# Kernel tuning notes

Measured on AMD Instinct MI355X. Metric: run time of the kernel, lower is better.

Reference implementation:

```python
import jax, jax.numpy as jnp
import numpy as np

B, N, M, C1, C2 = 16, 4096, 1024, 128, 256
MLP0, MLP1 = 256, 256
IN_CH = C1 + C2
EPS = 1e-5


def setup_inputs() -> dict:
    key = jax.random.key(0)
    ks = jax.random.split(key, 6)
    return {
        "xyz1": jax.random.normal(ks[0], (B, 3, N), jnp.float32),
        "xyz2": jax.random.normal(ks[1], (B, 3, M), jnp.float32),
        "points1": jax.random.normal(ks[2], (B, C1, N), jnp.float32),
        "points2": jax.random.normal(ks[3], (B, C2, M), jnp.float32),
        "W1": jax.random.normal(ks[4], (MLP0, IN_CH), jnp.float32) * (1.0 / np.sqrt(IN_CH)),
        "gamma1": jnp.ones((MLP0,), jnp.float32),
        "beta1": jnp.zeros((MLP0,), jnp.float32),
        "W2": jax.random.normal(ks[5], (MLP1, MLP0), jnp.float32) * (1.0 / np.sqrt(MLP0)),
        "gamma2": jnp.ones((MLP1,), jnp.float32),
        "beta2": jnp.zeros((MLP1,), jnp.float32),
    }


def _batchnorm(x, gamma, beta):
    # x: (B, N, C); normalize per channel over batch*length (training-mode BN, biased var)
    mean = jnp.mean(x, axis=(0, 1))
    var = jnp.mean((x - mean) ** 2, axis=(0, 1))
    return (x - mean) * jax.lax.rsqrt(var + EPS) * gamma + beta


def reference(xyz1, xyz2, points1, points2, W1, gamma1, beta1, W2, gamma2, beta2):
    p1 = jnp.swapaxes(xyz1, 1, 2)  # (B, N, 3)
    p2 = jnp.swapaxes(xyz2, 1, 2)  # (B, M, 3)
    # squared pairwise distances (B, N, M); squaring preserves 3-NN ordering,
    # and the original squares the euclidean dist before weighting anyway
    d2 = jnp.sum((p1[:, :, None, :] - p2[:, None, :, :]) ** 2, axis=-1)
    neg_d2, idx = jax.lax.top_k(-d2, 3)  # 3 smallest distances
    dist2 = jnp.maximum(-neg_d2, 1e-10)  # (B, N, 3)
    inv = 1.0 / dist2
    weight = inv / jnp.sum(inv, axis=-1, keepdims=True)  # (B, N, 3)
    f2 = jnp.swapaxes(points2, 1, 2)  # (B, M, C2)
    b, n, k = idx.shape
    gathered = jnp.take_along_axis(
        f2, idx.reshape(b, n * k)[:, :, None], axis=1
    ).reshape(b, n, k, -1)  # (B, N, 3, C2)
    interp = jnp.einsum("bnk,bnkc->bnc", weight, gathered)  # (B, N, C2)
    feat = jnp.concatenate([interp, jnp.swapaxes(points1, 1, 2)], axis=-1)  # (B, N, C1+C2)
    h = jnp.einsum("bnc,oc->bno", feat, W1)  # conv1d k=1, no bias
    h = jax.nn.relu(_batchnorm(h, gamma1, beta1))
    h = jnp.einsum("bnc,oc->bno", h, W2)
    h = jax.nn.relu(_batchnorm(h, gamma2, beta2))
    return jnp.swapaxes(h, 1, 2)  # (B, MLP1, N), channel-first like torch
```

## Files before the change

kernel.cpp:

```cpp
#include <hip/hip_runtime.h>

typedef unsigned short u16;
typedef unsigned int u32;

#define BB 16
#define NN 4096
#define MM 1024
#define C1V 128
#define C2V 256
#define EPSV 1e-5f
#define INV_CNT (1.0f/65536.0f)
#define NREP 32

typedef __attribute__((ext_vector_type(8))) short bf16x8;
typedef __attribute__((ext_vector_type(4))) float f32x4;

static __device__ __forceinline__ u16 f2b(float f) {
  u32 u = __float_as_uint(f);
  u32 r = (u + 0x7FFFu + ((u >> 16) & 1u)) >> 16;
  return (u16)r;
}
static __device__ __forceinline__ float b2f(u16 s) {
  return __uint_as_float(((u32)s) << 16);
}

#define GLD_LDS16(gp, lp)                                                      \
  __builtin_amdgcn_global_load_lds(                                            \
      (const __attribute__((address_space(1))) void*)(gp),                     \
      (__attribute__((address_space(3))) void*)(lp), 16, 0, 0)

__device__ __forceinline__ void tcast_tile64(const float* __restrict__ in,
                                             u16* __restrict__ out, int C,
                                             int P, int p0, int c0, int b,
                                             float (*tile)[33]) {
  int tx = threadIdx.x & 31, ty = threadIdx.x >> 5;
  const float* ib = in + (size_t)b * C * P;
  u16* ob = out + (size_t)b * P * C;
#pragma unroll
  for (int i = 0; i < 8; ++i)
    tile[ty + i * 8][tx] = ib[(size_t)(c0 + ty + i * 8) * P + p0 + tx];
  __syncthreads();
#pragma unroll
  for (int i = 0; i < 4; ++i) {
    int p = ty + i * 8;
    u32 v = (u32)f2b(tile[tx * 2][p]) | ((u32)f2b(tile[tx * 2 + 1][p]) << 16);
    *(u32*)&ob[(size_t)(p0 + p) * C + c0 + tx * 2] = v;
  }
}

__global__ __launch_bounds__(256) void prep_kernel(
    const float* __restrict__ xyz1, const float* __restrict__ xyz2,
    float* __restrict__ pd, int* __restrict__ pi,
    const float* __restrict__ points1, const float* __restrict__ points2,
    u16* __restrict__ p1t, u16* __restrict__ p2t,
    const float* __restrict__ W1, const float* __restrict__ W2,
    u16* __restrict__ W1b, u16* __restrict__ W2b,
    float* __restrict__ statsZero) {
  __shared__ float4 cand[256];
  __shared__ float tile[64][33];
  int bx = blockIdx.x;
  int t = threadIdx.x;

  if (bx < 512) {
    int c = bx & 3;
    int qt = (bx >> 2) & 7;
    int b = bx >> 5;
    const float* x2b = xyz2 + b * 3 * MM;
    {
      float x = x2b[c * 256 + t];
      float y = x2b[MM + c * 256 + t];
      float z = x2b[2 * MM + c * 256 + t];
      cand[t] = make_float4(x, y, z, x * x + y * y + z * z);
    }
    __syncthreads();
    const float* x1b = xyz1 + b * 3 * NN;
    int n0 = qt * 512 + t;
    int n1 = n0 + 256;
    float px0 = x1b[n0], py0 = x1b[NN + n0], pz0 = x1b[2 * NN + n0];
    float px1 = x1b[n1], py1 = x1b[NN + n1], pz1 = x1b[2 * NN + n1];
    const float INF = 3.4e38f;
    float k00 = INF, k01 = INF, k02 = INF;
    float k10 = INF, k11 = INF, k12 = INF;
    int j00 = 0, j01 = 0, j02 = 0;
    int j10 = 0, j11 = 0, j12 = 0;
#pragma unroll 8
    for (int m = 0; m < 256; ++m) {
      float4 cd = cand[m];
      {
        float dot = fmaf(px0, cd.x, fmaf(py0, cd.y, pz0 * cd.z));
        float key = fmaf(-2.0f, dot, cd.w);
        bool c0 = key < k00, c1 = key < k01, c2 = key < k02;
        k02 = c1 ? k01 : (c2 ? key : k02);
        j02 = c1 ? j01 : (c2 ? m : j02);
        k01 = c0 ? k00 : (c1 ? key : k01);
        j01 = c0 ? j00 : (c1 ? m : j01);
        k00 = c0 ? key : k00;
        j00 = c0 ? m : j00;
      }
      {
        float dot = fmaf(px1, cd.x, fmaf(py1, cd.y, pz1 * cd.z));
        float key = fmaf(-2.0f, dot, cd.w);
        bool c0 = key < k10, c1 = key < k11, c2 = key < k12;
        k12 = c1 ? k11 : (c2 ? key : k12);
        j12 = c1 ? j11 : (c2 ? m : j12);
        k11 = c0 ? k10 : (c1 ? key : k11);
        j11 = c0 ? j10 : (c1 ? m : j11);
        k10 = c0 ? key : k10;
        j10 = c0 ? m : j10;
      }
    }
    float pn0 = px0 * px0 + py0 * py0 + pz0 * pz0;
    float pn1 = px1 * px1 + py1 * py1 + pz1 * pz1;
    int gq0 = b * NN + n0;
    int gq1 = b * NN + n1;
    int base = c << 8;
    ((float4*)pd)[(size_t)c * 65536 + gq0] =
        make_float4(fmaxf(k00 + pn0, 1e-10f), fmaxf(k01 + pn0, 1e-10f),
                    fmaxf(k02 + pn0, 1e-10f), 0.0f);
    ((int4*)pi)[(size_t)c * 65536 + gq0] =
        make_int4(base + j00, base + j01, base + j02, 0);
    ((float4*)pd)[(size_t)c * 65536 + gq1] =
        make_float4(fmaxf(k10 + pn1, 1e-10f), fmaxf(k11 + pn1, 1e-10f),
                    fmaxf(k12 + pn1, 1e-10f), 0.0f);
    ((int4*)pi)[(size_t)c * 65536 + gq1] =
        make_int4(base + j10, base + j11, base + j12, 0);
  } else if (bx < 1152) {
    int i = (bx - 512) * 256 + t;
    if (i < 98304) W1b[i] = f2b(W1[i]);
    else if (i < 163840) W2b[i - 98304] = f2b(W2[i - 98304]);
  } else if (bx < 1184) {
    ((float4*)statsZero)[(bx - 1152) * 256 + t] =
        make_float4(0.f, 0.f, 0.f, 0.f);
  } else if (bx < 3232) {
    int local = bx - 1184;
    int pt = local & 31, ct = (local >> 5) & 3, b = local >> 7;
    tcast_tile64(points2, p2t, C2V, MM, pt * 32, ct * 64, b, tile);
  } else {
    int local = bx - 3232;
    int pt = local & 127, ct = (local >> 7) & 1, b = local >> 8;
    tcast_tile64(points1, p1t, C1V, NN, pt * 32, ct * 64, b, tile);
  }
}

template <int K, int NTILES, bool OUTB>
__global__ __launch_bounds__(256) void gemm_mfma(
    const u16* __restrict__ A, int lda, const u16* __restrict__ B, int ldb,
    void* __restrict__ out) {
  __shared__ u16 smem[16384];
  int t = threadIdx.x;
  int w = t >> 6, l = t & 63;
  int n0;
  if (NTILES > 0) {
    int p = blockIdx.x;
    int batch = ((p & 7) << 1) | ((p >> 3) & 1);
    int nt = p >> 4;
    n0 = (batch * NTILES + nt) * 128;
  } else {
    n0 = blockIdx.x * 128;
  }
  int o0 = blockIdx.y * 128;

  int wm = w & 1, wn = w >> 1;
  int lr = l >> 2, lc = l & 3;
  int q = l >> 4, m = l & 15;

  f32x4 acc[4][4] = {};
  u16* As = smem;
  u16* Bs = smem + 4096;

  const u16* arow = A + (size_t)n0 * lda;
  const u16* brow = B + (size_t)o0 * ldb;

#pragma unroll
  for (int kt = 0; kt < K; kt += 32) {
    __syncthreads();
#pragma unroll
    for (int r = 0; r < 2; ++r) {
      int row = r * 64 + w * 16 + lr;
      GLD_LDS16(arow + (size_t)row * lda + kt + lc * 8, As + row * 32 + lc * 8);
    }
#pragma unroll
    for (int r = 0; r < 2; ++r) {
      int row = r * 64 + w * 16 + lr;
      GLD_LDS16(brow + (size_t)row * ldb + kt + lc * 8, Bs + row * 32 + lc * 8);
    }
    __syncthreads();
    bf16x8 af[4], bf[4];
#pragma unroll
    for (int i = 0; i < 4; ++i)
      af[i] = *(const bf16x8*)(As + (wm * 64 + i * 16 + m) * 32 + q * 8);
#pragma unroll
    for (int j = 0; j < 4; ++j)
      bf[j] = *(const bf16x8*)(Bs + (wn * 64 + j * 16 + m) * 32 + q * 8);
#pragma unroll
    for (int i = 0; i < 4; ++i)
#pragma unroll
      for (int j = 0; j < 4; ++j)
        acc[i][j] =
            __builtin_amdgcn_mfma_f32_16x16x32_bf16(af[i], bf[j], acc[i][j], 0, 0, 0);
  }

  if (OUTB) {
    __syncthreads();
#pragma unroll
    for (int i = 0; i < 4; ++i)
#pragma unroll
      for (int reg = 0; reg < 4; ++reg) {
        int row = wm * 64 + i * 16 + q * 4 + reg;
#pragma unroll
        for (int j = 0; j < 4; ++j)
          smem[row * 128 + wn * 64 + j * 16 + m] = f2b(acc[i][j][reg]);
      }
    __syncthreads();
    u16* outp = (u16*)out;
    int rbase = w * 32 + (l >> 4);
    int seg = l & 15;
#pragma unroll
    for (int itr = 0; itr < 8; ++itr) {
      int row = rbase + itr * 4;
      uint4 v = *(const uint4*)(smem + row * 128 + seg * 8);
      *(uint4*)(outp + (size_t)(n0 + row) * 256 + o0 + seg * 8) = v;
    }
  } else {
#pragma unroll
    for (int i = 0; i < 4; ++i) {
      int gr = n0 + wm * 64 + i * 16 + q * 4;
#pragma unroll
      for (int reg = 0; reg < 4; ++reg)
#pragma unroll
        for (int j = 0; j < 4; ++j) {
          int gc = o0 + wn * 64 + j * 16 + m;
          ((float*)out)[(size_t)(gr + reg) * 256 + gc] = acc[i][j][reg];
        }
    }
  }
}

__global__ __launch_bounds__(256) void gemm1_64(
    const u16* __restrict__ A, const u16* __restrict__ B,
    u16* __restrict__ out, const u16* __restrict__ G,
    const float* __restrict__ pd, const int* __restrict__ pi,
    float* __restrict__ statsOut) {
  __shared__ __align__(16) u16 smem[16384];
  __shared__ float wsh[64][3];
  __shared__ int ish[64][3];
  int t = threadIdx.x;
  int w = t >> 6, l = t & 63;
  int p = blockIdx.x;
  int batch = ((p & 7) << 1) | ((p >> 3) & 1);
  int nt = p >> 4;
  int n0 = batch * NN + nt * 64;

  if (t < 64) {
    int gq = n0 + t;
    float4 d0 = ((const float4*)pd)[gq];
    int4 ii0 = ((const int4*)pi)[gq];
    float a0 = d0.x, a1 = d0.y, a2 = d0.z;
    int b0 = ii0.x, b1 = ii0.y, b2 = ii0.z;
#pragma unroll
    for (int c = 1; c < 4; ++c) {
      float4 dc = ((const float4*)pd)[(size_t)c * 65536 + gq];
      int4 ic = ((const int4*)pi)[(size_t)c * 65536 + gq];
      float kv[3] = {dc.x, dc.y, dc.z};
      int jv[3] = {ic.x, ic.y, ic.z};
#pragma unroll
      for (int j = 0; j < 3; ++j) {
        float key = kv[j];
        int idx = jv[j];
        bool c0 = key < a0, c1 = key < a1, c2 = key < a2;
        a2 = c1 ? a1 : (c2 ? key : a2);
        b2 = c1 ? b1 : (c2 ? idx : b2);
        a1 = c0 ? a0 : (c1 ? key : a1);
        b1 = c0 ? b0 : (c1 ? idx : b1);
        a0 = c0 ? key : a0;
        b0 = c0 ? idx : b0;
      }
    }
    float v0 = 1.0f / a0, v1 = 1.0f / a1, v2 = 1.0f / a2;
    float s = 1.0f / (v0 + v1 + v2);
    wsh[t][0] = v0 * s; wsh[t][1] = v1 * s; wsh[t][2] = v2 * s;
    ish[t][0] = b0;     ish[t][1] = b1;     ish[t][2] = b2;
  }

  int q = l >> 4, m = l & 15;
  int sr = l >> 2, lc = l & 3;

  f32x4 acc[4][4] = {};
  u16* As = smem;
  u16* Bs = smem + 2048;
  const u16* arow = A + (size_t)n0 * 128;

#pragma unroll
  for (int kt = 0; kt < 128; kt += 32) {
    __syncthreads();
    {
      int row = w * 16 + sr;
      GLD_LDS16(arow + (size_t)row * 128 + kt + lc * 8, As + row * 32 + lc * 8);
    }
#pragma unroll
    for (int r = 0; r < 4; ++r) {
      int row = r * 64 + w * 16 + sr;
      GLD_LDS16(B + (size_t)row * 384 + kt + lc * 8, Bs + row * 32 + lc * 8);
    }
    __syncthreads();
    bf16x8 af[4], bf[4];
#pragma unroll
    for (int i = 0; i < 4; ++i)
      af[i] = *(const bf16x8*)(As + (i * 16 + m) * 32 + q * 8);
#pragma unroll
    for (int j = 0; j < 4; ++j)
      bf[j] = *(const bf16x8*)(Bs + (w * 64 + j * 16 + m) * 32 + q * 8);
#pragma unroll
    for (int i = 0; i < 4; ++i)
#pragma unroll
      for (int j = 0; j < 4; ++j)
        acc[i][j] =
            __builtin_amdgcn_mfma_f32_16x16x32_bf16(af[i], bf[j], acc[i][j], 0, 0, 0);
  }

  __syncthreads();
  {
    int b = n0 >> 12;
    int rl = t >> 2, qt = t & 3;
    float w0 = wsh[rl][0], w1 = wsh[rl][1], w2 = wsh[rl][2];
    const u16* g0 = G + ((size_t)(b * 1024 + ish[rl][0])) * 256 + qt * 64;
    const u16* g1 = G + ((size_t)(b * 1024 + ish[rl][1])) * 256 + qt * 64;
    const u16* g2 = G + ((size_t)(b * 1024 + ish[rl][2])) * 256 + qt * 64;
    int r3 = rl & 7;
#pragma unroll
    for (int c8 = 0; c8 < 8; ++c8) {
      bf16x8 v0 = *(const bf16x8*)(g0 + c8 * 8);
      bf16x8 v1 = *(const bf16x8*)(g1 + c8 * 8);
      bf16x8 v2 = *(const bf16x8*)(g2 + c8 * 8);
      union { uint4 u; u16 s[8]; } o;
#pragma unroll
      for (int e = 0; e < 8; ++e) {
        float f = w0 * b2f((u16)v0[e]) + w1 * b2f((u16)v1[e]) +
                  w2 * b2f((u16)v2[e]);
        o.s[e] = f2b(f);
      }
      int ch = (qt * 8 + c8) ^ r3;
      *(uint4*)(smem + rl * 256 + ch * 8) = o.u;
    }
  }
  __syncthreads();
#pragma unroll
  for (int i = 0; i < 4; ++i)
#pragma unroll
    for (int reg = 0; reg < 4; ++reg) {
      int row = i * 16 + q * 4 + reg;
      int rx = row & 7;
#pragma unroll
      for (int j = 0; j < 4; ++j) {
        int col = w * 64 + j * 16 + m;
        int off = row * 256 + (((col >> 3) ^ rx) << 3) + (col & 7);
        acc[i][j][reg] += b2f(smem[off]);
      }
    }

  {
    int rep = blockIdx.x & (NREP - 1);
#pragma unroll
    for (int j = 0; j < 4; ++j) {
      float s = 0.0f, ss = 0.0f;
#pragma unroll
      for (int i = 0; i < 4; ++i)
#pragma unroll
        for (int reg = 0; reg < 4; ++reg) {
          float v = acc[i][j][reg];
          s += v;
          ss += v * v;
        }
      s += __shfl_down(s, 32); ss += __shfl_down(ss, 32);
      s += __shfl_down(s, 16); ss += __shfl_down(ss, 16);
      if (l < 16) {
        int c = w * 64 + j * 16 + l;
        atomicAdd(&statsOut[rep * 512 + c], s);
        atomicAdd(&statsOut[rep * 512 + 256 + c], ss);
      }
    }
  }

  __syncthreads();
#pragma unroll
  for (int i = 0; i < 4; ++i)
#pragma unroll
    for (int reg = 0; reg < 4; ++reg) {
      int row = i * 16 + q * 4 + reg;
#pragma unroll
      for (int j = 0; j < 4; ++j)
        smem[row * 256 + w * 64 + j * 16 + m] = f2b(acc[i][j][reg]);
    }
  __syncthreads();
  int rbase = t >> 5, seg = t & 31;
#pragma unroll
  for (int itr = 0; itr < 8; ++itr) {
    int row = rbase + itr * 8;
    uint4 v = *(const uint4*)(smem + row * 256 + seg * 8);
    *(uint4*)(out + (size_t)(n0 + row) * 256 + seg * 8) = v;
  }
}

__global__ __launch_bounds__(256) void gemm2_64(
    const u16* __restrict__ A, const u16* __restrict__ B,
    u16* __restrict__ out, float* __restrict__ statsOut,
    const float* __restrict__ statsInR, const float* __restrict__ gamma,
    const float* __restrict__ beta) {
  __shared__ __align__(16) u16 smem[16384];
  __shared__ float scA[256], shA[256];
  int t = threadIdx.x;
  int w = t >> 6, l = t & 63;
  int n0 = blockIdx.x * 64;

  {
    float s = 0.0f, qq = 0.0f;
#pragma unroll
    for (int r = 0; r < NREP; ++r) {
      s += statsInR[r * 512 + t];
      qq += statsInR[r * 512 + 256 + t];
    }
    float mean = s * INV_CNT;
    float var = qq * INV_CNT - mean * mean;
    float sc = rsqrtf(var + EPSV) * gamma[t];
    scA[t] = sc;
    shA[t] = beta[t] - mean * sc;
  }

  int q = l >> 4, m = l & 15;
  int sr = l >> 2, lc = l & 3;

  f32x4 acc[4][4] = {};
  u16* As = smem;
  u16* Bs = smem + 2048;
  const u16* arow = A + (size_t)n0 * 256;

#pragma unroll
  for (int kt = 0; kt < 256; kt += 32) {
    __syncthreads();
    {
      int row = w * 16 + sr;
      union { uint4 u; u16 s[8]; } v, o;
      v.u = *(const uint4*)(arow + (size_t)row * 256 + kt + lc * 8);
      int cb = kt + lc * 8;
#pragma unroll
      for (int j = 0; j < 8; ++j) {
        float f = fmaf(b2f(v.s[j]), scA[cb + j], shA[cb + j]);
        o.s[j] = f2b(fmaxf(f, 0.0f));
      }
      *(uint4*)(As + row * 32 + lc * 8) = o.u;
    }
#pragma unroll
    for (int r = 0; r < 4; ++r) {
      int row = r * 64 + w * 16 + sr;
      GLD_LDS16(B + (size_t)row * 256 + kt + lc * 8, Bs + row * 32 + lc * 8);
    }
    __syncthreads();
    bf16x8 af[4], bf[4];
#pragma unroll
    for (int i = 0; i < 4; ++i)
      af[i] = *(const bf16x8*)(As + (i * 16 + m) * 32 + q * 8);
#pragma unroll
    for (int j = 0; j < 4; ++j)
      bf[j] = *(const bf16x8*)(Bs + (w * 64 + j * 16 + m) * 32 + q * 8);
#pragma unroll
    for (int i = 0; i < 4; ++i)
#pragma unroll
      for (int j = 0; j < 4; ++j)
        acc[i][j] =
            __builtin_amdgcn_mfma_f32_16x16x32_bf16(af[i], bf[j], acc[i][j], 0, 0, 0);
  }

  {
    int rep = blockIdx.x & (NREP - 1);
#pragma unroll
    for (int j = 0; j < 4; ++j) {
      float s = 0.0f, ss = 0.0f;
#pragma unroll
      for (int i = 0; i < 4; ++i)
#pragma unroll
        for (int reg = 0; reg < 4; ++reg) {
          float v = acc[i][j][reg];
          s += v;
          ss += v * v;
        }
      s += __shfl_down(s, 32); ss += __shfl_down(ss, 32);
      s += __shfl_down(s, 16); ss += __shfl_down(ss, 16);
      if (l < 16) {
        int c = w * 64 + j * 16 + l;
        atomicAdd(&statsOut[rep * 512 + c], s);
        atomicAdd(&statsOut[rep * 512 + 256 + c], ss);
      }
    }
  }

  __syncthreads();
#pragma unroll
  for (int i = 0; i < 4; ++i)
#pragma unroll
    for (int reg = 0; reg < 4; ++reg) {
      int row = i * 16 + q * 4 + reg;
#pragma unroll
      for (int j = 0; j < 4; ++j)
        smem[row * 256 + w * 64 + j * 16 + m] = f2b(acc[i][j][reg]);
    }
  __syncthreads();
  int rbase = t >> 5, seg = t & 31;
#pragma unroll
  for (int itr = 0; itr < 8; ++itr) {
    int row = rbase + itr * 8;
    uint4 v = *(const uint4*)(smem + row * 256 + seg * 8);
    *(uint4*)(out + (size_t)(n0 + row) * 256 + seg * 8) = v;
  }
}

__global__ __launch_bounds__(256) void bn2t_kernel(
    const u16* __restrict__ h2, const float* __restrict__ statsR,
    const float* __restrict__ gamma, const float* __restrict__ beta,
    float* __restrict__ out) {
  __shared__ float tile[64][65];
  __shared__ float sS[64], sH[64];
  int t = threadIdx.x;
  int n0 = blockIdx.x * 64, c0 = blockIdx.y * 64, b = blockIdx.z;
  if (t < 64) {
    int c = c0 + t;
    float s = 0.0f, qq = 0.0f;
#pragma unroll
    for (int r = 0; r < NREP; ++r) {
      s += statsR[r * 512 + c];
      qq += statsR[r * 512 + 256 + c];
    }
    float mean = s * INV_CNT;
    float var = qq * INV_CNT - mean * mean;
    float sc = rsqrtf(var + EPSV) * gamma[c];
    sS[t] = sc;
    sH[t] = beta[c] - mean * sc;
  }
  __syncthreads();
  int tx = t & 15, ty = t >> 4;
#pragma unroll
  for (int i = 0; i < 4; ++i) {
    int n = ty + i * 16;
    uint2 v = *(const uint2*)(h2 + ((size_t)b * NN + n0 + n) * 256 + c0 + tx * 4);
    int c = tx * 4;
    tile[n][c + 0] = fmaxf(fmaf(b2f((u16)(v.x & 0xffff)), sS[c + 0], sH[c + 0]), 0.0f);
    tile[n][c + 1] = fmaxf(fmaf(b2f((u16)(v.x >> 16)),    sS[c + 1], sH[c + 1]), 0.0f);
    tile[n][c + 2] = fmaxf(fmaf(b2f((u16)(v.y & 0xffff)), sS[c + 2], sH[c + 2]), 0.0f);
    tile[n][c + 3] = fmaxf(fmaf(b2f((u16)(v.y >> 16)),    sS[c + 3], sH[c + 3]), 0.0f);
  }
  __syncthreads();
#pragma unroll
  for (int i = 0; i < 4; ++i) {
    int c = ty + i * 16;
    int nq = tx * 4;
    float4 o4 = make_float4(tile[nq + 0][c], tile[nq + 1][c],
                            tile[nq + 2][c], tile[nq + 3][c]);
    *(float4*)(out + ((size_t)(b * 256 + c0 + c)) * NN + n0 + nq) = o4;
  }
}

extern "C" void kernel_launch(void* const* d_in, const int* in_sizes, int n_in,
                              void* d_out, int out_size, void* d_ws,
                              size_t ws_size, hipStream_t stream) {
  const float* xyz1    = (const float*)d_in[0];
  const float* xyz2    = (const float*)d_in[1];
  const float* points1 = (const float*)d_in[2];
  const float* points2 = (const float*)d_in[3];
  const float* W1      = (const float*)d_in[4];
  const float* gamma1  = (const float*)d_in[5];
  const float* beta1   = (const float*)d_in[6];
  const float* W2      = (const float*)d_in[7];
  const float* gamma2  = (const float*)d_in[8];
  const float* beta2   = (const float*)d_in[9];

  char* ws = (char*)d_ws;
  float* stats1R = (float*)(ws + 0);
  float* stats2R = (float*)(ws + 65536);
  u16*   W1b     = (u16*)(ws + 131072);
  u16*   W2b     = (u16*)(ws + 327680);
  u16*   p2t     = (u16*)(ws + 458752);
  u16*   p1t     = (u16*)(ws + 8847360);
  u16*   G       = (u16*)(ws + 25624576);
  u16*   h2b     = (u16*)(ws + 34013184);
  float* pd      = (float*)(ws + 67567616);
  int*   pi      = (int*)(ws + 71761920);
  u16*   h1b     = (u16*)d_out;
  float* out     = (float*)d_out;

  prep_kernel<<<7328, 256, 0, stream>>>(xyz1, xyz2, pd, pi, points1, points2,
                                        p1t, p2t, W1, W2, W1b, W2b, stats1R);
  gemm_mfma<256, 8, true><<<dim3(128, 2), 256, 0, stream>>>(p2t, 256, W1b, 384,
                                                            G);
  gemm1_64<<<1024, 256, 0, stream>>>(p1t, W1b + 256, h1b, G, pd, pi, stats1R);
  gemm2_64<<<1024, 256, 0, stream>>>(h1b, W2b, h2b, stats2R, stats1R, gamma1,
                                     beta1);
  bn2t_kernel<<<dim3(64, 4, 16), 256, 0, stream>>>(h2b, stats2R, gamma2,
                                                   beta2, out);
}
```

Measured before the change: 221.8 us.

## Move KNN search blocks from prep kernel into the first GEMM launch

The 3-nearest-neighbour search blocks leave the prep kernel and run as extra blocks (blockIdx.x >= 128) of the first MFMA GEMM launch, reusing its shared memory for the candidate array. The GEMM grid grows from 128x2 to 384x2 to cover the 512 KNN blocks. KNN only depends on xyz inputs, so it can overlap with the p2t·W1 GEMM instead of sharing the prep launch with the cast/transpose work. The risk is that KNN blocks and GEMM blocks compete for CUs and that the prep kernel, now lighter, no longer hides the KNN compute.

After: 225.2 us. About the same (+1.5%).

```diff
diff --git a/kernel.cpp b/kernel.cpp
--- a/kernel.cpp
+++ b/kernel.cpp
@@ -49,22 +49,48 @@
 }
 
 __global__ __launch_bounds__(256) void prep_kernel(
-    const float* __restrict__ xyz1, const float* __restrict__ xyz2,
-    float* __restrict__ pd, int* __restrict__ pi,
     const float* __restrict__ points1, const float* __restrict__ points2,
     u16* __restrict__ p1t, u16* __restrict__ p2t,
     const float* __restrict__ W1, const float* __restrict__ W2,
     u16* __restrict__ W1b, u16* __restrict__ W2b,
     float* __restrict__ statsZero) {
-  __shared__ float4 cand[256];
   __shared__ float tile[64][33];
   int bx = blockIdx.x;
   int t = threadIdx.x;
 
-  if (bx < 512) {
-    int c = bx & 3;
-    int qt = (bx >> 2) & 7;
-    int b = bx >> 5;
+  if (bx < 640) {
+    int i = bx * 256 + t;
+    if (i < 98304) W1b[i] = f2b(W1[i]);
+    else if (i < 163840) W2b[i - 98304] = f2b(W2[i - 98304]);
+  } else if (bx < 672) {
+    ((float4*)statsZero)[(bx - 640) * 256 + t] =
+        make_float4(0.f, 0.f, 0.f, 0.f);
+  } else if (bx < 2720) {
+    int local = bx - 672;
+    int pt = local & 31, ct = (local >> 5) & 3, b = local >> 7;
+    tcast_tile64(points2, p2t, C2V, MM, pt * 32, ct * 64, b, tile);
+  } else {
+    int local = bx - 2720;
+    int pt = local & 127, ct = (local >> 7) & 1, b = local >> 8;
+    tcast_tile64(points1, p1t, C1V, NN, pt * 32, ct * 64, b, tile);
+  }
+}
+
+template <int K, int NTILES, bool OUTB, bool KNN>
+__global__ __launch_bounds__(256) void gemm_mfma(
+    const u16* __restrict__ A, int lda, const u16* __restrict__ B, int ldb,
+    void* __restrict__ out, const float* __restrict__ xyz1,
+    const float* __restrict__ xyz2, float* __restrict__ pd,
+    int* __restrict__ pi) {
+  __shared__ __align__(16) u16 smem[16384];
+  int t = threadIdx.x;
+
+  if (KNN && blockIdx.x >= 128) {
+    float4* cand = (float4*)smem;
+    int id = (int)(blockIdx.x - 128) | ((int)blockIdx.y << 8);
+    int c = id & 3;
+    int qt = (id >> 2) & 7;
+    int b = id >> 5;
     const float* x2b = xyz2 + b * 3 * MM;
     {
       float x = x2b[c * 256 + t];
@@ -124,30 +150,9 @@
                     fmaxf(k12 + pn1, 1e-10f), 0.0f);
     ((int4*)pi)[(size_t)c * 65536 + gq1] =
         make_int4(base + j10, base + j11, base + j12, 0);
-  } else if (bx < 1152) {
-    int i = (bx - 512) * 256 + t;
-    if (i < 98304) W1b[i] = f2b(W1[i]);
-    else if (i < 163840) W2b[i - 98304] = f2b(W2[i - 98304]);
-  } else if (bx < 1184) {
-    ((float4*)statsZero)[(bx - 1152) * 256 + t] =
-        make_float4(0.f, 0.f, 0.f, 0.f);
-  } else if (bx < 3232) {
-    int local = bx - 1184;
-    int pt = local & 31, ct = (local >> 5) & 3, b = local >> 7;
-    tcast_tile64(points2, p2t, C2V, MM, pt * 32, ct * 64, b, tile);
-  } else {
-    int local = bx - 3232;
-    int pt = local & 127, ct = (local >> 7) & 1, b = local >> 8;
-    tcast_tile64(points1, p1t, C1V, NN, pt * 32, ct * 64, b, tile);
-  }
-}
-
-template <int K, int NTILES, bool OUTB>
-__global__ __launch_bounds__(256) void gemm_mfma(
-    const u16* __restrict__ A, int lda, const u16* __restrict__ B, int ldb,
-    void* __restrict__ out) {
-  __shared__ u16 smem[16384];
-  int t = threadIdx.x;
+    return;
+  }
+
   int w = t >> 6, l = t & 63;
   int n0;
   if (NTILES > 0) {
@@ -586,10 +591,10 @@
   u16*   h1b     = (u16*)d_out;
   float* out     = (float*)d_out;
 
-  prep_kernel<<<7328, 256, 0, stream>>>(xyz1, xyz2, pd, pi, points1, points2,
-                                        p1t, p2t, W1, W2, W1b, W2b, stats1R);
-  gemm_mfma<256, 8, true><<<dim3(128, 2), 256, 0, stream>>>(p2t, 256, W1b, 384,
-                                                            G);
+  prep_kernel<<<6816, 256, 0, stream>>>(points1, points2, p1t, p2t, W1, W2,
+                                        W1b, W2b, stats1R);
+  gemm_mfma<256, 8, true, true><<<dim3(384, 2), 256, 0, stream>>>(
+      p2t, 256, W1b, 384, G, xyz1, xyz2, pd, pi);
   gemm1_64<<<1024, 256, 0, stream>>>(p1t, W1b + 256, h1b, G, pd, pi, stats1R);
   gemm2_64<<<1024, 256, 0, stream>>>(h1b, W2b, h2b, stats2R, stats1R, gamma1,
                                      beta1);
```

## Double-buffer LDS tiles in gemm1 and gemm2 to overlap loads with MFMA

Applied to the files above, without the earlier changes.

Both GEMM kernels now keep two LDS buffers for the A and B K-slices. The next slice is prefetched while MFMAs run on the current one, which cuts each K step from two barriers to one. In gemm2 the BN+ReLU transform of the next A slice is applied after the MFMAs so its global load latency is hidden. The cost is more LDS per block (40KB vs 32KB) and more registers, which may reduce occupancy.

New measurement: 219.4 us. Within noise of the previous version (-1.1%).

```diff
diff --git a/kernel.cpp b/kernel.cpp
--- a/kernel.cpp
+++ b/kernel.cpp
@@ -241,7 +241,7 @@
     u16* __restrict__ out, const u16* __restrict__ G,
     const float* __restrict__ pd, const int* __restrict__ pi,
     float* __restrict__ statsOut) {
-  __shared__ __align__(16) u16 smem[16384];
+  __shared__ __align__(16) u16 smem[20480];
   __shared__ float wsh[64][3];
   __shared__ int ish[64][3];
   int t = threadIdx.x;
@@ -286,39 +286,52 @@
   int sr = l >> 2, lc = l & 3;
 
   f32x4 acc[4][4] = {};
-  u16* As = smem;
-  u16* Bs = smem + 2048;
+  u16* Asb[2] = {smem, smem + 2048};
+  u16* Bsb[2] = {smem + 4096, smem + 12288};
   const u16* arow = A + (size_t)n0 * 128;
 
-#pragma unroll
-  for (int kt = 0; kt < 128; kt += 32) {
-    __syncthreads();
-    {
+  {
+    int row = w * 16 + sr;
+    GLD_LDS16(arow + (size_t)row * 128 + lc * 8, Asb[0] + row * 32 + lc * 8);
+#pragma unroll
+    for (int r = 0; r < 4; ++r) {
+      int row2 = r * 64 + w * 16 + sr;
+      GLD_LDS16(B + (size_t)row2 * 384 + lc * 8, Bsb[0] + row2 * 32 + lc * 8);
+    }
+  }
+  __syncthreads();
+
+#pragma unroll
+  for (int it = 0; it < 4; ++it) {
+    const int cur = it & 1, nxt = cur ^ 1;
+    if (it < 3) {
+      int kt = (it + 1) * 32;
       int row = w * 16 + sr;
-      GLD_LDS16(arow + (size_t)row * 128 + kt + lc * 8, As + row * 32 + lc * 8);
-    }
-#pragma unroll
-    for (int r = 0; r < 4; ++r) {
-      int row = r * 64 + w * 16 + sr;
-      GLD_LDS16(B + (size_t)row * 384 + kt + lc * 8, Bs + row * 32 + lc * 8);
-    }
-    __syncthreads();
+      GLD_LDS16(arow + (size_t)row * 128 + kt + lc * 8,
+                Asb[nxt] + row * 32 + lc * 8);
+#pragma unroll
+      for (int r = 0; r < 4; ++r) {
+        int row2 = r * 64 + w * 16 + sr;
+        GLD_LDS16(B + (size_t)row2 * 384 + kt + lc * 8,
+                  Bsb[nxt] + row2 * 32 + lc * 8);
+      }
+    }
     bf16x8 af[4], bf[4];
 #pragma unroll
     for (int i = 0; i < 4; ++i)
-      af[i] = *(const bf16x8*)(As + (i * 16 + m) * 32 + q * 8);
+      af[i] = *(const bf16x8*)(Asb[cur] + (i * 16 + m) * 32 + q * 8);
 #pragma unroll
     for (int j = 0; j < 4; ++j)
-      bf[j] = *(const bf16x8*)(Bs + (w * 64 + j * 16 + m) * 32 + q * 8);
+      bf[j] = *(const bf16x8*)(Bsb[cur] + (w * 64 + j * 16 + m) * 32 + q * 8);
 #pragma unroll
     for (int i = 0; i < 4; ++i)
 #pragma unroll
       for (int j = 0; j < 4; ++j)
         acc[i][j] =
             __builtin_amdgcn_mfma_f32_16x16x32_bf16(af[i], bf[j], acc[i][j], 0, 0, 0);
-  }
-
-  __syncthreads();
+    __syncthreads();
+  }
+
   {
     int b = n0 >> 12;
     int rl = t >> 2, qt = t & 3;
@@ -406,7 +419,7 @@
     u16* __restrict__ out, float* __restrict__ statsOut,
     const float* __restrict__ statsInR, const float* __restrict__ gamma,
     const float* __restrict__ beta) {
-  __shared__ __align__(16) u16 smem[16384];
+  __shared__ __align__(16) u16 smem[20480];
   __shared__ float scA[256], shA[256];
   int t = threadIdx.x;
   int w = t >> 6, l = t & 63;
@@ -425,49 +438,75 @@
     scA[t] = sc;
     shA[t] = beta[t] - mean * sc;
   }
+  __syncthreads();
 
   int q = l >> 4, m = l & 15;
   int sr = l >> 2, lc = l & 3;
 
   f32x4 acc[4][4] = {};
-  u16* As = smem;
-  u16* Bs = smem + 2048;
+  u16* Asb[2] = {smem, smem + 2048};
+  u16* Bsb[2] = {smem + 4096, smem + 12288};
   const u16* arow = A + (size_t)n0 * 256;
-
-#pragma unroll
-  for (int kt = 0; kt < 256; kt += 32) {
-    __syncthreads();
-    {
-      int row = w * 16 + sr;
-      union { uint4 u; u16 s[8]; } v, o;
-      v.u = *(const uint4*)(arow + (size_t)row * 256 + kt + lc * 8);
-      int cb = kt + lc * 8;
-#pragma unroll
-      for (int j = 0; j < 8; ++j) {
-        float f = fmaf(b2f(v.s[j]), scA[cb + j], shA[cb + j]);
-        o.s[j] = f2b(fmaxf(f, 0.0f));
-      }
-      *(uint4*)(As + row * 32 + lc * 8) = o.u;
-    }
+  int arowoff = (w * 16 + sr) * 256 + lc * 8;
+  int aldsoff = (w * 16 + sr) * 32 + lc * 8;
+
+  {
+    union { uint4 u; u16 s[8]; } v, o;
+    v.u = *(const uint4*)(arow + arowoff);
 #pragma unroll
     for (int r = 0; r < 4; ++r) {
-      int row = r * 64 + w * 16 + sr;
-      GLD_LDS16(B + (size_t)row * 256 + kt + lc * 8, Bs + row * 32 + lc * 8);
-    }
-    __syncthreads();
+      int row2 = r * 64 + w * 16 + sr;
+      GLD_LDS16(B + (size_t)row2 * 256 + lc * 8, Bsb[0] + row2 * 32 + lc * 8);
+    }
+    int cb = lc * 8;
+#pragma unroll
+    for (int j = 0; j < 8; ++j) {
+      float f = fmaf(b2f(v.s[j]), scA[cb + j], shA[cb + j]);
+      o.s[j] = f2b(fmaxf(f, 0.0f));
+    }
+    *(uint4*)(Asb[0] + aldsoff) = o.u;
+  }
+  __syncthreads();
+
+#pragma unroll
+  for (int it = 0; it < 8; ++it) {
+    const int cur = it & 1, nxt = cur ^ 1;
+    union { uint4 u; u16 s[8]; } an;
+    if (it < 7) {
+      int kt = (it + 1) * 32;
+      an.u = *(const uint4*)(arow + arowoff + kt);
+#pragma unroll
+      for (int r = 0; r < 4; ++r) {
+        int row2 = r * 64 + w * 16 + sr;
+        GLD_LDS16(B + (size_t)row2 * 256 + kt + lc * 8,
+                  Bsb[nxt] + row2 * 32 + lc * 8);
+      }
+    }
     bf16x8 af[4], bf[4];
 #pragma unroll
     for (int i = 0; i < 4; ++i)
-      af[i] = *(const bf16x8*)(As + (i * 16 + m) * 32 + q * 8);
+      af[i] = *(const bf16x8*)(Asb[cur] + (i * 16 + m) * 32 + q * 8);
 #pragma unroll
     for (int j = 0; j < 4; ++j)
-      bf[j] = *(const bf16x8*)(Bs + (w * 64 + j * 16 + m) * 32 + q * 8);
+      bf[j] = *(const bf16x8*)(Bsb[cur] + (w * 64 + j * 16 + m) * 32 + q * 8);
 #pragma unroll
     for (int i = 0; i < 4; ++i)
 #pragma unroll
       for (int j = 0; j < 4; ++j)
         acc[i][j] =
             __builtin_amdgcn_mfma_f32_16x16x32_bf16(af[i], bf[j], acc[i][j], 0, 0, 0);
+    if (it < 7) {
+      int kt = (it + 1) * 32;
+      int cb = kt + lc * 8;
+      union { uint4 u; u16 s[8]; } o;
+#pragma unroll
+      for (int j = 0; j < 8; ++j) {
+        float f = fmaf(b2f(an.s[j]), scA[cb + j], shA[cb + j]);
+        o.s[j] = f2b(fmaxf(f, 0.0f));
+      }
+      *(uint4*)(Asb[nxt] + aldsoff) = o.u;
+    }
+    __syncthreads();
   }
 
   {
```
